# Kernel optimization log

Measured on AMD Instinct MI355X. Metric: run time of the kernel, lower is better.

Reference implementation:

```python
import jax, jax.numpy as jnp
import numpy as np

# Coarse-to-fine lossless 3D segmentation (Seg3dLossless), batch=1, C=1.
RES = [17, 33, 65, 129]          # odd resolutions, stride (RF-1)/(R-1) is integral
RF = RES[-1]
B_MIN, B_MAX = -1.0, 1.0
BAL = 0.5                        # balance_value
N_CONFLICT_ITERS = 2             # fixed unroll of the data-dependent while-loop


def _mlp(pts, w1, b1, w2, b2, w3, b3):
    # query_func: occupancy MLP on normalized (x,y,z) points -> [N]
    h = jax.nn.relu(pts @ w1 + b1)
    h = jax.nn.relu(h @ w2 + b2)
    return jax.nn.sigmoid(h @ w3 + b3)[..., 0]


def _eval_grid(R, w1, b1, w2, b2, w3, b3):
    # batch_eval with align_corners=False: coords2D = (coord + 0.5)/RF, mapped to [B_MIN,B_MAX]
    s = (RF - 1) // (R - 1)
    c = jnp.arange(R, dtype=jnp.float32) * s                 # final-res integer coords
    p = (c + 0.5) / RF * (B_MAX - B_MIN) + B_MIN
    zz, yy, xx = jnp.meshgrid(p, p, p, indexing='ij')        # [D,H,W]
    pts = jnp.stack([xx, yy, zz], axis=-1).reshape(-1, 3)    # (x,y,z) order
    return _mlp(pts, w1, b1, w2, b2, w3, b3).reshape(R, R, R)


def _resize(x, R):
    # trilinear, align_corners=True: out index j -> in coord j*(in-1)/(out-1)
    c = jnp.linspace(0.0, x.shape[0] - 1.0, R)
    zz, yy, xx = jnp.meshgrid(c, c, c, indexing='ij')
    return jax.scipy.ndimage.map_coordinates(x, [zz, yy, xx], order=1, mode='nearest')


def _dilate(m):
    # smooth_conv3x3 (mean filter) followed by >0 == 3x3x3 binary dilation
    f = jax.lax.reduce_window(m.astype(jnp.float32), 0.0, jax.lax.max,
                              (3, 3, 3), (1, 1, 1), 'SAME')
    return f > 0.0


def setup_inputs() -> dict:
    key = jax.random.key(0)
    k1, k2, k3 = jax.random.split(key, 3)
    H = 64
    return {
        'w1': jax.random.normal(k1, (3, H), jnp.float32) * 0.8,
        'b1': jnp.zeros((H,), jnp.float32),
        'w2': jax.random.normal(k2, (H, H), jnp.float32) * (1.0 / np.sqrt(H)),
        'b2': jnp.zeros((H,), jnp.float32),
        'w3': jax.random.normal(k3, (H, 1), jnp.float32) * (1.0 / np.sqrt(H)),
        'b3': jnp.zeros((1,), jnp.float32),
    }


def reference(w1, b1, w2, b2, w3, b3):
    params = (w1, b1, w2, b2, w3, b3)
    # level 0: dense eval on the coarse grid
    occ = _eval_grid(RES[0], *params)                        # [R0,R0,R0]
    s0 = (RF - 1) // (RES[0] - 1)
    calculated = jnp.zeros((RF, RF, RF), bool).at[::s0, ::s0, ::s0].set(True)

    for R in RES[1:]:
        s = (RF - 1) // (R - 1)
        valid = _resize((occ > BAL).astype(jnp.float32), R)  # no-grad mask path
        occ_i = _resize(occ, R)                              # differentiable interp
        boundary = _dilate((valid > 0.0) & (valid < 1.0))
        calc_l = calculated[::s, ::s, ::s]
        boundary = boundary & (~calc_l)                      # skip already-evaluated voxels
        occ_true = _eval_grid(R, *params)                    # query_func at this level
        occ = jnp.where(boundary, occ_true, occ_i)           # scatter of occupancys_topk
        calc_l = calc_l | boundary
        # conflict resolution: re-query 3^3 neighbors of sign-flip voxels
        conflict = boundary & ((occ_i - BAL) * (occ_true - BAL) < 0.0)
        for _ in range(N_CONFLICT_ITERS):
            nbr = _dilate(conflict) & (~calc_l)
            occ_prev = occ
            occ = jnp.where(nbr, occ_true, occ)
            calc_l = calc_l | nbr
            conflict = nbr & ((occ_prev - BAL) * (occ_true - BAL) < 0.0)
        calculated = calculated.at[::s, ::s, ::s].set(calc_l)

    return occ[None, None]                                   # (1, 1, D, H, W)
```

## Files before the change

kernel.cpp:

```cpp
#include <hip/hip_runtime.h>

#define HH 64

static __global__ void k_prep_w2t(const float* __restrict__ w2, float* __restrict__ w2t){
  int t = blockIdx.x * 256 + threadIdx.x;
  w2t[t] = w2[(t & 63) * HH + (t >> 6)];
}

__device__ __forceinline__ void mlp_pair(
    const float* __restrict__ sw1,
    const float* __restrict__ sw2t,
    const float* __restrict__ b2, const float* __restrict__ w3,
    const float* __restrict__ b3,
    float xA, float yA, float zA, float xB, float yB, float zB,
    float& outA, float& outB)
{
  const int ibase = ((threadIdx.x & 63) >> 5) * 32;
  float h1a[32], h1b[32];
  #pragma unroll
  for (int k = 0; k < 32; k += 4){
    const float4 wx = *(const float4*)&sw1[      ibase + k];
    const float4 wy = *(const float4*)&sw1[ 64 + ibase + k];
    const float4 wz = *(const float4*)&sw1[128 + ibase + k];
    const float4 bb = *(const float4*)&sw1[192 + ibase + k];
    h1a[k+0] = fmaxf(fmaf(xA,wx.x,fmaf(yA,wy.x,fmaf(zA,wz.x,bb.x))),0.f);
    h1a[k+1] = fmaxf(fmaf(xA,wx.y,fmaf(yA,wy.y,fmaf(zA,wz.y,bb.y))),0.f);
    h1a[k+2] = fmaxf(fmaf(xA,wx.z,fmaf(yA,wy.z,fmaf(zA,wz.z,bb.z))),0.f);
    h1a[k+3] = fmaxf(fmaf(xA,wx.w,fmaf(yA,wy.w,fmaf(zA,wz.w,bb.w))),0.f);
    h1b[k+0] = fmaxf(fmaf(xB,wx.x,fmaf(yB,wy.x,fmaf(zB,wz.x,bb.x))),0.f);
    h1b[k+1] = fmaxf(fmaf(xB,wx.y,fmaf(yB,wy.y,fmaf(zB,wz.y,bb.y))),0.f);
    h1b[k+2] = fmaxf(fmaf(xB,wx.z,fmaf(yB,wy.z,fmaf(zB,wz.z,bb.z))),0.f);
    h1b[k+3] = fmaxf(fmaf(xB,wx.w,fmaf(yB,wy.w,fmaf(zB,wz.w,bb.w))),0.f);
  }
  float oa = b3[0], ob = oa;
  #pragma unroll 1
  for (int j = 0; j < HH; ++j){
    const float4* wrow = (const float4*)&sw2t[j*HH + ibase];
    float a0 = 0.f, a1 = 0.f, c0 = 0.f, c1 = 0.f;
    #pragma unroll
    for (int q = 0; q < 8; q += 2){
      const float4 w0 = wrow[q];
      const float4 w1q = wrow[q+1];
      a0 = fmaf(h1a[4*q+0], w0.x, a0);
      a0 = fmaf(h1a[4*q+1], w0.y, a0);
      a0 = fmaf(h1a[4*q+2], w0.z, a0);
      a0 = fmaf(h1a[4*q+3], w0.w, a0);
      a1 = fmaf(h1a[4*q+4], w1q.x, a1);
      a1 = fmaf(h1a[4*q+5], w1q.y, a1);
      a1 = fmaf(h1a[4*q+6], w1q.z, a1);
      a1 = fmaf(h1a[4*q+7], w1q.w, a1);
      c0 = fmaf(h1b[4*q+0], w0.x, c0);
      c0 = fmaf(h1b[4*q+1], w0.y, c0);
      c0 = fmaf(h1b[4*q+2], w0.z, c0);
      c0 = fmaf(h1b[4*q+3], w0.w, c0);
      c1 = fmaf(h1b[4*q+4], w1q.x, c1);
      c1 = fmaf(h1b[4*q+5], w1q.y, c1);
      c1 = fmaf(h1b[4*q+6], w1q.z, c1);
      c1 = fmaf(h1b[4*q+7], w1q.w, c1);
    }
    float accA = a0 + a1, accB = c0 + c1;
    accA += __shfl_xor(accA, 32);
    accB += __shfl_xor(accB, 32);
    const float bj = b2[j], wj = w3[j];
    oa = fmaf(fmaxf(accA + bj, 0.f), wj, oa);
    ob = fmaf(fmaxf(accB + bj, 0.f), wj, ob);
  }
  outA = 1.f / (1.f + expf(-oa));
  outB = 1.f / (1.f + expf(-ob));
}

#define STAGE_WEIGHTS()                                            \
  __shared__ float sw1[4*HH];                                      \
  __shared__ float sw2t[HH*HH];                                    \
  {                                                                \
    const int t0 = threadIdx.x;                                    \
    if (t0 < 3*HH) sw1[t0] = w1[t0];                               \
    else sw1[t0] = b1[t0 - 3*HH];                                  \
    const float4* s4 = (const float4*)w2t;                         \
    float4* d4 = (float4*)sw2t;                                    \
    for (int i4 = t0; i4 < HH*HH/4; i4 += 256) d4[i4] = s4[i4];    \
    __syncthreads();                                               \
  }

__device__ __forceinline__ float mlp_eval_s(
    const float* __restrict__ w1, const float* __restrict__ b1,
    const float* __restrict__ w2t, const float* __restrict__ b2,
    const float* __restrict__ w3, const float* __restrict__ b3,
    float x, float y, float z)
{
  float h1[HH];
  #pragma unroll
  for (int i = 0; i < HH; ++i){
    float v = b1[i];
    v = fmaf(x, w1[i],        v);
    v = fmaf(y, w1[HH + i],   v);
    v = fmaf(z, w1[2*HH + i], v);
    h1[i] = fmaxf(v, 0.0f);
  }
  float o = b3[0];
  #pragma unroll 2
  for (int j = 0; j < HH; ++j){
    float acc = b2[j];
    const float* wr = &w2t[j*HH];
    #pragma unroll
    for (int k = 0; k < HH; ++k) acc = fmaf(h1[k], wr[k], acc);
    o = fmaf(fmaxf(acc, 0.0f), w3[j], o);
  }
  return 1.0f / (1.0f + expf(-o));
}

static __global__ __launch_bounds__(256)
__attribute__((amdgpu_waves_per_eu(4,4)))
void k_eval_mlp(
    const float* __restrict__ w1, const float* __restrict__ b1,
    const float* __restrict__ w2t, const float* __restrict__ b2,
    const float* __restrict__ w3, const float* __restrict__ b3,
    float* __restrict__ out, unsigned char* __restrict__ calc1,
    int R, int s)
{
  STAGE_WEIGHTS();
  const unsigned int n = (unsigned int)R * (unsigned int)R * (unsigned int)R;
  const int lane = threadIdx.x & 63;
  const int wid = threadIdx.x >> 6;
  const unsigned int base = blockIdx.x * 256u + (unsigned int)(wid * 64 + (lane & 31));
  const unsigned int pidA = base < n ? base : (n - 1u);
  const unsigned int pB = base + 32u;
  const unsigned int pidB = pB < n ? pB : (n - 1u);
  const float inv129x2 = 2.0f / 129.0f;
  unsigned int cA = pidA % (unsigned int)R, rA = pidA / (unsigned int)R;
  unsigned int cB = pidB % (unsigned int)R, rB = pidB / (unsigned int)R;
  const float xA = ((float)(cA * (unsigned int)s) + 0.5f) * inv129x2 - 1.0f;
  const float yA = ((float)((rA % (unsigned int)R) * (unsigned int)s) + 0.5f) * inv129x2 - 1.0f;
  const float zA = ((float)((rA / (unsigned int)R) * (unsigned int)s) + 0.5f) * inv129x2 - 1.0f;
  const float xB = ((float)(cB * (unsigned int)s) + 0.5f) * inv129x2 - 1.0f;
  const float yB = ((float)((rB % (unsigned int)R) * (unsigned int)s) + 0.5f) * inv129x2 - 1.0f;
  const float zB = ((float)((rB / (unsigned int)R) * (unsigned int)s) + 0.5f) * inv129x2 - 1.0f;
  float oA, oB;
  mlp_pair(sw1, sw2t, b2, w3, b3, xA, yA, zA, xB, yB, zB, oA, oB);
  if ((threadIdx.x & 63) < 32){
    if (base < n){ out[pidA] = oA; if (calc1) calc1[pidA] = 1; }
    if (pB < n)  { out[pidB] = oB; if (calc1) calc1[pidB] = 1; }
  }
}

static __global__ __launch_bounds__(256, 4) void k_eval_dense_mism(
    const float* __restrict__ w1, const float* __restrict__ b1,
    const float* __restrict__ w2t, const float* __restrict__ b2,
    const float* __restrict__ w3, const float* __restrict__ b3,
    const float* __restrict__ occ_i,
    float* __restrict__ out, unsigned char* __restrict__ mism,
    int R, int s)
{
  const unsigned int n = (unsigned int)R * (unsigned int)R * (unsigned int)R;
  unsigned int pid = blockIdx.x * 256u + threadIdx.x;
  if (pid >= n) return;
  const unsigned int c = pid % (unsigned int)R;
  const unsigned int r = pid / (unsigned int)R;
  const unsigned int b = r % (unsigned int)R;
  const unsigned int a = r / (unsigned int)R;
  const float inv129x2 = 2.0f / 129.0f;
  const float x = ((float)(c * (unsigned int)s) + 0.5f) * inv129x2 - 1.0f;
  const float y = ((float)(b * (unsigned int)s) + 0.5f) * inv129x2 - 1.0f;
  const float z = ((float)(a * (unsigned int)s) + 0.5f) * inv129x2 - 1.0f;
  float ot = mlp_eval_s(w1, b1, w2t, b2, w3, b3, x, y, z);
  out[pid] = ot;
  mism[pid] = ((occ_i[pid] - 0.5f) * (ot - 0.5f) < 0.0f) ? (unsigned char)1 : (unsigned char)0;
}

static __global__ __launch_bounds__(256)
__attribute__((amdgpu_waves_per_eu(4,4)))
void k_eval_sparse(
    const float* __restrict__ w1, const float* __restrict__ b1,
    const float* __restrict__ w2t, const float* __restrict__ b2,
    const float* __restrict__ w3, const float* __restrict__ b3,
    const int* __restrict__ idxl, const unsigned int* __restrict__ cnt,
    const float* __restrict__ occ_i,
    float* __restrict__ out, unsigned char* __restrict__ mism,
    int R, int s, unsigned int n)
{
  unsigned int count = *cnt;
  if (count > n) count = n;
  if (blockIdx.x * 256u >= count) return;
  STAGE_WEIGHTS();
  const int lane = threadIdx.x & 63;
  const int wid = threadIdx.x >> 6;
  const unsigned int slotA = blockIdx.x * 256u + (unsigned int)(wid * 64 + (lane & 31));
  const unsigned int slotB = slotA + 32u;
  const bool vA = slotA < count, vB = slotB < count;
  const unsigned int pidA = (unsigned int)idxl[vA ? slotA : 0];
  const unsigned int pidB = (unsigned int)idxl[vB ? slotB : 0];
  const float inv129x2 = 2.0f / 129.0f;
  unsigned int cA = pidA % (unsigned int)R, rA = pidA / (unsigned int)R;
  unsigned int cB = pidB % (unsigned int)R, rB = pidB / (unsigned int)R;
  const float xA = ((float)(cA * (unsigned int)s) + 0.5f) * inv129x2 - 1.0f;
  const float yA = ((float)((rA % (unsigned int)R) * (unsigned int)s) + 0.5f) * inv129x2 - 1.0f;
  const float zA = ((float)((rA / (unsigned int)R) * (unsigned int)s) + 0.5f) * inv129x2 - 1.0f;
  const float xB = ((float)(cB * (unsigned int)s) + 0.5f) * inv129x2 - 1.0f;
  const float yB = ((float)((rB % (unsigned int)R) * (unsigned int)s) + 0.5f) * inv129x2 - 1.0f;
  const float zB = ((float)((rB / (unsigned int)R) * (unsigned int)s) + 0.5f) * inv129x2 - 1.0f;
  float oA, oB;
  mlp_pair(sw1, sw2t, b2, w3, b3, xA, yA, zA, xB, yB, zB, oA, oB);
  if ((threadIdx.x & 63) < 32){
    if (vA){
      out[pidA] = oA;
      mism[pidA] = ((occ_i[pidA] - 0.5f) * (oA - 0.5f) < 0.0f) ? (unsigned char)1 : (unsigned char)0;
    }
    if (vB){
      out[pidB] = oB;
      mism[pidB] = ((occ_i[pidB] - 0.5f) * (oB - 0.5f) < 0.0f) ? (unsigned char)1 : (unsigned char)0;
    }
  }
}

static __global__ __launch_bounds__(256) void k_resize_b0(
    const float* __restrict__ prev,
    const unsigned char* __restrict__ calc_prev,
    float* __restrict__ occ_i, float* __restrict__ occ_out,
    unsigned char* __restrict__ bnd0, unsigned char* __restrict__ calc_out,
    unsigned char* __restrict__ confA, unsigned char* __restrict__ confB,
    unsigned char* __restrict__ upd, int R, int Rp)
{
  const unsigned int n = (unsigned int)R * (unsigned int)R * (unsigned int)R;
  unsigned int gid = blockIdx.x * 256u + threadIdx.x;
  if (gid >= n) return;
  int c = (int)(gid % (unsigned int)R);
  unsigned int r = gid / (unsigned int)R;
  int b = (int)(r % (unsigned int)R);
  int a = (int)(r / (unsigned int)R);
  int a0 = a >> 1, da = a & 1;
  int b0i = b >> 1, db = b & 1;
  int c0 = c >> 1, dc = c & 1;
  float sum = 0.0f;
  int cnt = 0;
  const int tot = (da + 1) * (db + 1) * (dc + 1);
  for (int dz = 0; dz <= da; ++dz)
    for (int dy = 0; dy <= db; ++dy)
      for (int dx = 0; dx <= dc; ++dx){
        float v = prev[((unsigned int)(a0 + dz) * (unsigned int)Rp + (unsigned int)(b0i + dy)) * (unsigned int)Rp + (unsigned int)(c0 + dx)];
        sum += v;
        cnt += (v > 0.5f) ? 1 : 0;
      }
  float oi = sum / (float)tot;
  occ_i[gid] = oi;
  occ_out[gid] = oi;
  bnd0[gid] = (cnt > 0 && cnt < tot) ? 1 : 0;
  calc_out[gid] = ((da | db | dc) == 0)
      ? calc_prev[((unsigned int)a0 * (unsigned int)Rp + (unsigned int)b0i) * (unsigned int)Rp + (unsigned int)c0]
      : (unsigned char)0;
  confA[gid] = 0; confB[gid] = 0; upd[gid] = 0;
}

static __global__ __launch_bounds__(256) void k_resize_boundary(
    const float* __restrict__ prev, const float* __restrict__ occ_true,
    const unsigned char* __restrict__ calc_prev,
    float* __restrict__ occ_i, float* __restrict__ occ_out,
    unsigned char* __restrict__ bnd0,
    unsigned char* __restrict__ mism, unsigned char* __restrict__ calc_out,
    int R, int Rp)
{
  const unsigned int n = (unsigned int)R * (unsigned int)R * (unsigned int)R;
  unsigned int gid = blockIdx.x * 256u + threadIdx.x;
  if (gid >= n) return;
  int c = (int)(gid % (unsigned int)R);
  unsigned int r = gid / (unsigned int)R;
  int b = (int)(r % (unsigned int)R);
  int a = (int)(r / (unsigned int)R);
  int a0 = a >> 1, da = a & 1;
  int b0i = b >> 1, db = b & 1;
  int c0 = c >> 1, dc = c & 1;
  float sum = 0.0f;
  int cnt = 0;
  const int tot = (da + 1) * (db + 1) * (dc + 1);
  for (int dz = 0; dz <= da; ++dz)
    for (int dy = 0; dy <= db; ++dy)
      for (int dx = 0; dx <= dc; ++dx){
        float v = prev[((unsigned int)(a0 + dz) * (unsigned int)Rp + (unsigned int)(b0i + dy)) * (unsigned int)Rp + (unsigned int)(c0 + dx)];
        sum += v;
        cnt += (v > 0.5f) ? 1 : 0;
      }
  float oi = sum / (float)tot;
  occ_i[gid] = oi;
  occ_out[gid] = oi;
  bnd0[gid] = (cnt > 0 && cnt < tot) ? 1 : 0;
  mism[gid] = ((oi - 0.5f) * (occ_true[gid] - 0.5f) < 0.0f) ? 1 : 0;
  calc_out[gid] = ((da | db | dc) == 0)
      ? calc_prev[((unsigned int)a0 * (unsigned int)Rp + (unsigned int)b0i) * (unsigned int)Rp + (unsigned int)c0]
      : (unsigned char)0;
}

static __global__ __launch_bounds__(512) void k_dil7_tiled(
    const unsigned char* __restrict__ in, unsigned char* __restrict__ outp,
    unsigned int* __restrict__ bcnt, int R, int T)
{
  __shared__ unsigned char s0[14*14*14];
  __shared__ unsigned char s1[14*14*8];
  __shared__ unsigned char s2[14*8*8];
  __shared__ unsigned int wc[8];
  const int tile = blockIdx.x;
  const int tz = tile / (T*T);
  const int ty = (tile / T) % T;
  const int tx = tile % T;
  const int bz = tz*8 - 3, by = ty*8 - 3, bx = tx*8 - 3;
  const int t = threadIdx.x;
  for (int i = t; i < 14*14*14; i += 512){
    int lz = i / 196, rr = i % 196, ly = rr / 14, lx = rr % 14;
    int gz = bz + lz, gy = by + ly, gx = bx + lx;
    unsigned char v = 0;
    if (gz >= 0 && gz < R && gy >= 0 && gy < R && gx >= 0 && gx < R)
      v = in[((unsigned int)gz * (unsigned int)R + (unsigned int)gy) * (unsigned int)R + (unsigned int)gx];
    s0[i] = v;
  }
  __syncthreads();
  for (int i = t; i < 14*14*8; i += 512){
    int lz = i / 112, rr = i % 112, ly = rr / 8, lx = rr % 8;
    const unsigned char* p = &s0[lz*196 + ly*14 + lx];
    s1[i] = (unsigned char)(p[0]|p[1]|p[2]|p[3]|p[4]|p[5]|p[6]);
  }
  __syncthreads();
  for (int i = t; i < 14*8*8; i += 512){
    int lz = i / 64, rr = i % 64, ly = rr / 8, lx = rr % 8;
    const unsigned char* p = &s1[lz*112 + ly*8 + lx];
    s2[i] = (unsigned char)(p[0]|p[8]|p[16]|p[24]|p[32]|p[40]|p[48]);
  }
  __syncthreads();
  int lz = t >> 6, ly = (t >> 3) & 7, lx = t & 7;
  const unsigned char* p = &s2[lz*64 + ly*8 + lx];
  int m = p[0]|p[64]|p[128]|p[192]|p[256]|p[320]|p[384];
  int gz = tz*8 + lz, gy = ty*8 + ly, gx = tx*8 + lx;
  bool inb = (gz < R) && (gy < R) && (gx < R);
  if (inb) outp[((unsigned int)gz * (unsigned int)R + (unsigned int)gy) * (unsigned int)R + (unsigned int)gx]
      = (unsigned char)(m ? 1 : 0);
  unsigned long long bm = __ballot(inb && m);
  int w = t >> 6;
  if ((t & 63) == 0) wc[w] = (unsigned int)__popcll(bm);
  __syncthreads();
  if (t == 0) bcnt[blockIdx.x] = wc[0]+wc[1]+wc[2]+wc[3]+wc[4]+wc[5]+wc[6]+wc[7];
}

static __global__ __launch_bounds__(1024) void k_scan(
    unsigned int* __restrict__ bcnt, unsigned int nb, unsigned int* __restrict__ total)
{
  __shared__ unsigned int part[1024];
  const unsigned int t = threadIdx.x;
  const unsigned int chunk = (nb + 1023u) / 1024u;
  const unsigned int beg = t * chunk;
  const unsigned int end = (beg + chunk < nb) ? (beg + chunk) : nb;
  unsigned int s = 0;
  for (unsigned int i = beg; i < end; ++i) s += bcnt[i];
  part[t] = s;
  __syncthreads();
  for (int offd = 1; offd < 1024; offd <<= 1){
    unsigned int v = (t >= (unsigned int)offd) ? part[t - offd] : 0u;
    __syncthreads();
    part[t] += v;
    __syncthreads();
  }
  unsigned int run = (t == 0) ? 0u : part[t - 1];
  for (unsigned int i = beg; i < end; ++i){
    unsigned int v = bcnt[i];
    bcnt[i] = run;
    run += v;
  }
  if (t == 1023) *total = part[1023];
}

static __global__ __launch_bounds__(512) void k_scatter_tiled(
    const unsigned char* __restrict__ cand, const unsigned int* __restrict__ boff,
    int* __restrict__ idxl, int R, int T)
{
  __shared__ unsigned int wbase[8];
  const int tile = blockIdx.x;
  const int tz = tile / (T*T), ty = (tile / T) % T, tx = tile % T;
  const int t = threadIdx.x;
  int lz = t >> 6, ly = (t >> 3) & 7, lx = t & 7;
  int gz = tz*8 + lz, gy = ty*8 + ly, gx = tx*8 + lx;
  bool inb = (gz < R) && (gy < R) && (gx < R);
  int gid = inb ? (int)(((unsigned int)gz * (unsigned int)R + (unsigned int)gy) * (unsigned int)R + (unsigned int)gx) : 0;
  bool pred = inb && (cand[gid] != 0);
  unsigned long long m = __ballot(pred);
  int w = t >> 6, lane = t & 63;
  if (lane == 0) wbase[w] = (unsigned int)__popcll(m);
  __syncthreads();
  if (t == 0){
    unsigned int run = boff[blockIdx.x];
    for (int i = 0; i < 8; ++i){ unsigned int v = wbase[i]; wbase[i] = run; run += v; }
  }
  __syncthreads();
  if (pred){
    int pre = __popcll(m & ((1ull << lane) - 1ull));
    idxl[wbase[w] + (unsigned int)pre] = gid;
  }
}

static __global__ __launch_bounds__(256) void k_dilate_sparse(
    const int* __restrict__ idxl, const unsigned int* __restrict__ cnt,
    const unsigned char* __restrict__ src, const unsigned char* __restrict__ mism,
    unsigned char* __restrict__ calc, unsigned char* __restrict__ conf_out,
    unsigned char* __restrict__ upd, int R, int final_step,
    const float* __restrict__ occ_true, float* __restrict__ occ_out,
    unsigned int n)
{
  unsigned int count = *cnt;
  if (count > n) count = n;
  for (unsigned int slot = blockIdx.x * 256u + threadIdx.x; slot < count;
       slot += gridDim.x * 256u){
    int gid = idxl[slot];
    int c = gid % R;
    int r = gid / R;
    int b = r % R;
    int a = r / R;
    int m = 0;
    for (int dz = -1; dz <= 1; ++dz){
      int az = a + dz; if (az < 0 || az >= R) continue;
      for (int dy = -1; dy <= 1; ++dy){
        int by = b + dy; if (by < 0 || by >= R) continue;
        for (int dx = -1; dx <= 1; ++dx){
          int cx = c + dx; if (cx < 0 || cx >= R) continue;
          m |= src[(az * R + by) * R + cx];
        }
      }
    }
    unsigned char nb = (m && !calc[gid]) ? (unsigned char)1 : (unsigned char)0;
    conf_out[gid] = (nb && mism[gid]) ? (unsigned char)1 : (unsigned char)0;
    unsigned char u = upd[gid];
    if (nb){ calc[gid] = 1; if (!u){ upd[gid] = 1; u = 1; } }
    if (final_step && u) occ_out[gid] = occ_true[gid];
  }
}

static __global__ __launch_bounds__(256) void k_dilate_step(
    const unsigned char* __restrict__ src, const unsigned char* __restrict__ mism,
    unsigned char* __restrict__ calc, unsigned char* __restrict__ conf_out,
    unsigned char* __restrict__ upd, int R, int first, int final_step,
    const float* __restrict__ occ_true, float* __restrict__ occ_out)
{
  const unsigned int n = (unsigned int)R * (unsigned int)R * (unsigned int)R;
  unsigned int gid = blockIdx.x * 256u + threadIdx.x;
  if (gid >= n) return;
  int c = (int)(gid % (unsigned int)R);
  unsigned int r = gid / (unsigned int)R;
  int b = (int)(r % (unsigned int)R);
  int a = (int)(r / (unsigned int)R);
  int m = 0;
  for (int dz = -1; dz <= 1; ++dz){
    int az = a + dz; if (az < 0 || az >= R) continue;
    for (int dy = -1; dy <= 1; ++dy){
      int by = b + dy; if (by < 0 || by >= R) continue;
      for (int dx = -1; dx <= 1; ++dx){
        int cx = c + dx; if (cx < 0 || cx >= R) continue;
        m |= src[((unsigned int)az * (unsigned int)R + (unsigned int)by) * (unsigned int)R + (unsigned int)cx];
      }
    }
  }
  unsigned char nb = (m && !calc[gid]) ? (unsigned char)1 : (unsigned char)0;
  if (nb) calc[gid] = 1;
  conf_out[gid] = (nb && mism[gid]) ? (unsigned char)1 : (unsigned char)0;
  unsigned char u;
  if (first){ u = nb; upd[gid] = nb; }
  else { u = upd[gid]; if (nb && !u){ upd[gid] = 1; u = 1; } }
  if (final_step && u) occ_out[gid] = occ_true[gid];
}

extern "C" void kernel_launch(void* const* d_in, const int* in_sizes, int n_in,
                              void* d_out, int out_size, void* d_ws, size_t ws_size,
                              hipStream_t stream)
{
  const float* w1 = (const float*)d_in[0];
  const float* b1 = (const float*)d_in[1];
  const float* w2 = (const float*)d_in[2];
  const float* b2 = (const float*)d_in[3];
  const float* w3 = (const float*)d_in[4];
  const float* b3 = (const float*)d_in[5];
  float* out = (float*)d_out;

  const int NF = 129 * 129 * 129;
  const int NP = 65 * 65 * 65;
  char* ws = (char*)d_ws;
  size_t off = 0;
  auto alloc = [&](size_t bytes) -> void* {
    void* p = (void*)(ws + off);
    off += (bytes + 255) & ~(size_t)255;
    return p;
  };
  float* f_true  = (float*)alloc((size_t)NF * 4);
  float* f_occi  = (float*)alloc((size_t)NF * 4);
  float* f_prevA = (float*)alloc((size_t)NP * 4);
  float* f_prevB = (float*)alloc((size_t)NP * 4);
  float* f_w2t   = (float*)alloc((size_t)HH * HH * 4);
  int*   i_idx   = (int*)alloc((size_t)NF * 4);
  unsigned int* u_cnt  = (unsigned int*)alloc(256);
  unsigned int* u_bcnt = (unsigned int*)alloc(8448 * 4);
  unsigned char* b_b0    = (unsigned char*)alloc(NF);
  unsigned char* b_mism  = (unsigned char*)alloc(NF);
  unsigned char* b_confA = (unsigned char*)alloc(NF);
  unsigned char* b_confB = (unsigned char*)alloc(NF);
  unsigned char* b_calcA = (unsigned char*)alloc(NF);
  unsigned char* b_calcB = (unsigned char*)alloc(NF);
  unsigned char* b_upd   = (unsigned char*)alloc(NF);
  unsigned char* b_cand  = (unsigned char*)alloc(NF);
  (void)ws_size;

  k_prep_w2t<<<16, 256, 0, stream>>>(w2, f_w2t);

  {
    int R = 17, s = 8;
    int n = R * R * R;
    int blocks = (n + 255) / 256;
    k_eval_mlp<<<blocks, 256, 0, stream>>>(w1, b1, f_w2t, b2, w3, b3, f_prevA, b_calcA, R, s);
  }

  int Rp = 17;
  float* prev = f_prevA;
  unsigned char* calcP = b_calcA;
  unsigned char* calcC = b_calcB;
  for (int li = 1; li <= 3; ++li){
    int R = 2 * Rp - 1;
    int s = 128 / (R - 1);
    unsigned int n = (unsigned int)R * (unsigned int)R * (unsigned int)R;
    int blocks = (int)((n + 255u) / 256u);
    float* occ_out = (li == 3) ? out : ((prev == f_prevA) ? f_prevB : f_prevA);

    if (R == 33){
      k_eval_mlp<<<blocks, 256, 0, stream>>>(w1, b1, f_w2t, b2, w3, b3, f_true, (unsigned char*)nullptr, R, s);
      k_resize_boundary<<<blocks, 256, 0, stream>>>(prev, f_true, calcP, f_occi, occ_out, b_b0, b_mism, calcC, R, Rp);
      k_dilate_step<<<blocks, 256, 0, stream>>>(b_b0,    b_mism, calcC, b_confA, b_upd, R, 1, 0, f_true, occ_out);
      k_dilate_step<<<blocks, 256, 0, stream>>>(b_confA, b_mism, calcC, b_confB, b_upd, R, 0, 0, f_true, occ_out);
      k_dilate_step<<<blocks, 256, 0, stream>>>(b_confB, b_mism, calcC, b_confA, b_upd, R, 0, 1, f_true, occ_out);
    } else if (R == 65){
      k_resize_b0<<<blocks, 256, 0, stream>>>(prev, calcP, f_occi, occ_out, b_b0, calcC,
                                              b_confA, b_confB, b_upd, R, Rp);
      k_eval_dense_mism<<<blocks, 256, 0, stream>>>(w1, b1, f_w2t, b2, w3, b3, f_occi, f_true, b_mism, R, s);
      k_dilate_step<<<blocks, 256, 0, stream>>>(b_b0,    b_mism, calcC, b_confA, b_upd, R, 1, 0, f_true, occ_out);
      k_dilate_step<<<blocks, 256, 0, stream>>>(b_confA, b_mism, calcC, b_confB, b_upd, R, 0, 0, f_true, occ_out);
      k_dilate_step<<<blocks, 256, 0, stream>>>(b_confB, b_mism, calcC, b_confA, b_upd, R, 0, 1, f_true, occ_out);
    } else {
      const int T = (R + 7) / 8;
      const int tblocks = T * T * T;
      k_resize_b0<<<blocks, 256, 0, stream>>>(prev, calcP, f_occi, occ_out, b_b0, calcC,
                                              b_confA, b_confB, b_upd, R, Rp);
      k_dil7_tiled<<<tblocks, 512, 0, stream>>>(b_b0, b_cand, u_bcnt, R, T);
      k_scan<<<1, 1024, 0, stream>>>(u_bcnt, (unsigned int)tblocks, u_cnt);
      k_scatter_tiled<<<tblocks, 512, 0, stream>>>(b_cand, u_bcnt, i_idx, R, T);
      k_eval_sparse<<<blocks, 256, 0, stream>>>(
          w1, b1, f_w2t, b2, w3, b3, i_idx, u_cnt, f_occi, f_true, b_mism, R, s, n);
      int sblocks = blocks < 4096 ? blocks : 4096;
      k_dilate_sparse<<<sblocks, 256, 0, stream>>>(i_idx, u_cnt, b_b0,    b_mism, calcC, b_confA, b_upd, R, 0, f_true, occ_out, n);
      k_dilate_sparse<<<sblocks, 256, 0, stream>>>(i_idx, u_cnt, b_confA, b_mism, calcC, b_confB, b_upd, R, 0, f_true, occ_out, n);
      k_dilate_sparse<<<sblocks, 256, 0, stream>>>(i_idx, u_cnt, b_confB, b_mism, calcC, b_confA, b_upd, R, 1, f_true, occ_out, n);
    }

    prev = occ_out;
    unsigned char* tmpc = calcP; calcP = calcC; calcC = tmpc;
    Rp = R;
  }
  (void)in_sizes; (void)n_in; (void)out_size;
}
```

Measured before the change: 321.4 us.

## Fuse three conflict-dilation passes into one shared-memory tiled kernel per level

```diff
diff --git a/kernel.cpp b/kernel.cpp
--- a/kernel.cpp
+++ b/kernel.cpp
@@ -82,33 +82,6 @@
     __syncthreads();                                               \
   }
 
-__device__ __forceinline__ float mlp_eval_s(
-    const float* __restrict__ w1, const float* __restrict__ b1,
-    const float* __restrict__ w2t, const float* __restrict__ b2,
-    const float* __restrict__ w3, const float* __restrict__ b3,
-    float x, float y, float z)
-{
-  float h1[HH];
-  #pragma unroll
-  for (int i = 0; i < HH; ++i){
-    float v = b1[i];
-    v = fmaf(x, w1[i],        v);
-    v = fmaf(y, w1[HH + i],   v);
-    v = fmaf(z, w1[2*HH + i], v);
-    h1[i] = fmaxf(v, 0.0f);
-  }
-  float o = b3[0];
-  #pragma unroll 2
-  for (int j = 0; j < HH; ++j){
-    float acc = b2[j];
-    const float* wr = &w2t[j*HH];
-    #pragma unroll
-    for (int k = 0; k < HH; ++k) acc = fmaf(h1[k], wr[k], acc);
-    o = fmaf(fmaxf(acc, 0.0f), w3[j], o);
-  }
-  return 1.0f / (1.0f + expf(-o));
-}
-
 static __global__ __launch_bounds__(256)
 __attribute__((amdgpu_waves_per_eu(4,4)))
 void k_eval_mlp(
@@ -141,30 +114,6 @@
     if (base < n){ out[pidA] = oA; if (calc1) calc1[pidA] = 1; }
     if (pB < n)  { out[pidB] = oB; if (calc1) calc1[pidB] = 1; }
   }
-}
-
-static __global__ __launch_bounds__(256, 4) void k_eval_dense_mism(
-    const float* __restrict__ w1, const float* __restrict__ b1,
-    const float* __restrict__ w2t, const float* __restrict__ b2,
-    const float* __restrict__ w3, const float* __restrict__ b3,
-    const float* __restrict__ occ_i,
-    float* __restrict__ out, unsigned char* __restrict__ mism,
-    int R, int s)
-{
-  const unsigned int n = (unsigned int)R * (unsigned int)R * (unsigned int)R;
-  unsigned int pid = blockIdx.x * 256u + threadIdx.x;
-  if (pid >= n) return;
-  const unsigned int c = pid % (unsigned int)R;
-  const unsigned int r = pid / (unsigned int)R;
-  const unsigned int b = r % (unsigned int)R;
-  const unsigned int a = r / (unsigned int)R;
-  const float inv129x2 = 2.0f / 129.0f;
-  const float x = ((float)(c * (unsigned int)s) + 0.5f) * inv129x2 - 1.0f;
-  const float y = ((float)(b * (unsigned int)s) + 0.5f) * inv129x2 - 1.0f;
-  const float z = ((float)(a * (unsigned int)s) + 0.5f) * inv129x2 - 1.0f;
-  float ot = mlp_eval_s(w1, b1, w2t, b2, w3, b3, x, y, z);
-  out[pid] = ot;
-  mism[pid] = ((occ_i[pid] - 0.5f) * (ot - 0.5f) < 0.0f) ? (unsigned char)1 : (unsigned char)0;
 }
 
 static __global__ __launch_bounds__(256)
@@ -217,8 +166,7 @@
     const unsigned char* __restrict__ calc_prev,
     float* __restrict__ occ_i, float* __restrict__ occ_out,
     unsigned char* __restrict__ bnd0, unsigned char* __restrict__ calc_out,
-    unsigned char* __restrict__ confA, unsigned char* __restrict__ confB,
-    unsigned char* __restrict__ upd, int R, int Rp)
+    int R, int Rp)
 {
   const unsigned int n = (unsigned int)R * (unsigned int)R * (unsigned int)R;
   unsigned int gid = blockIdx.x * 256u + threadIdx.x;
@@ -247,7 +195,6 @@
   calc_out[gid] = ((da | db | dc) == 0)
       ? calc_prev[((unsigned int)a0 * (unsigned int)Rp + (unsigned int)b0i) * (unsigned int)Rp + (unsigned int)c0]
       : (unsigned char)0;
-  confA[gid] = 0; confB[gid] = 0; upd[gid] = 0;
 }
 
 static __global__ __launch_bounds__(256) void k_resize_boundary(
@@ -392,73 +339,95 @@
   }
 }
 
-static __global__ __launch_bounds__(256) void k_dilate_sparse(
-    const int* __restrict__ idxl, const unsigned int* __restrict__ cnt,
-    const unsigned char* __restrict__ src, const unsigned char* __restrict__ mism,
-    unsigned char* __restrict__ calc, unsigned char* __restrict__ conf_out,
-    unsigned char* __restrict__ upd, int R, int final_step,
-    const float* __restrict__ occ_true, float* __restrict__ occ_out,
-    unsigned int n)
-{
-  unsigned int count = *cnt;
-  if (count > n) count = n;
-  for (unsigned int slot = blockIdx.x * 256u + threadIdx.x; slot < count;
-       slot += gridDim.x * 256u){
-    int gid = idxl[slot];
-    int c = gid % R;
-    int r = gid / R;
-    int b = r % R;
-    int a = r / R;
+static __global__ __launch_bounds__(512) void k_dilate3_tiled(
+    const unsigned char* __restrict__ b0,
+    const unsigned char* __restrict__ mism,
+    unsigned char* __restrict__ calc,
+    const float* __restrict__ occ_true,
+    float* __restrict__ occ_out,
+    int R, int T)
+{
+  __shared__ unsigned char sC[14*14*14];
+  __shared__ unsigned char sD[14*14*14];
+  __shared__ unsigned char sK[14*14*14];
+  __shared__ unsigned char sM[14*14*14];
+  __shared__ int s_any;
+  const int tile = blockIdx.x;
+  const int tz = tile / (T*T), ty = (tile / T) % T, tx = tile % T;
+  const int bz = tz*8 - 3, by = ty*8 - 3, bx = tx*8 - 3;
+  const int t = threadIdx.x;
+  if (t == 0) s_any = 0;
+  __syncthreads();
+  int any = 0;
+  for (int i = t; i < 2744; i += 512){
+    int lz = i / 196, rr = i % 196, ly = rr / 14, lx = rr % 14;
+    int gz = bz + lz, gy = by + ly, gx = bx + lx;
+    bool in = (gz >= 0 && gz < R && gy >= 0 && gy < R && gx >= 0 && gx < R);
+    unsigned int g = in ? (((unsigned int)gz * (unsigned int)R + (unsigned int)gy) * (unsigned int)R + (unsigned int)gx) : 0u;
+    unsigned char v0 = in ? b0[g] : (unsigned char)0;
+    sC[i] = v0; any |= v0;
+    sK[i] = in ? calc[g] : (unsigned char)1;
+    sM[i] = in ? mism[g] : (unsigned char)0;
+  }
+  if (any) s_any = 1;
+  __syncthreads();
+  if (!s_any) return;
+
+  const int clz = 3 + (t >> 6), cly = 3 + ((t >> 3) & 7), clx = 3 + (t & 7);
+  const int cp = clz*196 + cly*14 + clx;
+  const unsigned char calc0 = sK[cp];
+  __syncthreads();
+
+  for (int i = t; i < 1728; i += 512){
+    int lz = i / 144 + 1, rr = i % 144, ly = rr / 12 + 1, lx = rr % 12 + 1;
+    int p = lz*196 + ly*14 + lx;
     int m = 0;
-    for (int dz = -1; dz <= 1; ++dz){
-      int az = a + dz; if (az < 0 || az >= R) continue;
-      for (int dy = -1; dy <= 1; ++dy){
-        int by = b + dy; if (by < 0 || by >= R) continue;
-        for (int dx = -1; dx <= 1; ++dx){
-          int cx = c + dx; if (cx < 0 || cx >= R) continue;
-          m |= src[(az * R + by) * R + cx];
-        }
-      }
-    }
-    unsigned char nb = (m && !calc[gid]) ? (unsigned char)1 : (unsigned char)0;
-    conf_out[gid] = (nb && mism[gid]) ? (unsigned char)1 : (unsigned char)0;
-    unsigned char u = upd[gid];
-    if (nb){ calc[gid] = 1; if (!u){ upd[gid] = 1; u = 1; } }
-    if (final_step && u) occ_out[gid] = occ_true[gid];
-  }
-}
-
-static __global__ __launch_bounds__(256) void k_dilate_step(
-    const unsigned char* __restrict__ src, const unsigned char* __restrict__ mism,
-    unsigned char* __restrict__ calc, unsigned char* __restrict__ conf_out,
-    unsigned char* __restrict__ upd, int R, int first, int final_step,
-    const float* __restrict__ occ_true, float* __restrict__ occ_out)
-{
-  const unsigned int n = (unsigned int)R * (unsigned int)R * (unsigned int)R;
-  unsigned int gid = blockIdx.x * 256u + threadIdx.x;
-  if (gid >= n) return;
-  int c = (int)(gid % (unsigned int)R);
-  unsigned int r = gid / (unsigned int)R;
-  int b = (int)(r % (unsigned int)R);
-  int a = (int)(r / (unsigned int)R);
-  int m = 0;
-  for (int dz = -1; dz <= 1; ++dz){
-    int az = a + dz; if (az < 0 || az >= R) continue;
-    for (int dy = -1; dy <= 1; ++dy){
-      int by = b + dy; if (by < 0 || by >= R) continue;
-      for (int dx = -1; dx <= 1; ++dx){
-        int cx = c + dx; if (cx < 0 || cx >= R) continue;
-        m |= src[((unsigned int)az * (unsigned int)R + (unsigned int)by) * (unsigned int)R + (unsigned int)cx];
-      }
-    }
-  }
-  unsigned char nb = (m && !calc[gid]) ? (unsigned char)1 : (unsigned char)0;
-  if (nb) calc[gid] = 1;
-  conf_out[gid] = (nb && mism[gid]) ? (unsigned char)1 : (unsigned char)0;
-  unsigned char u;
-  if (first){ u = nb; upd[gid] = nb; }
-  else { u = upd[gid]; if (nb && !u){ upd[gid] = 1; u = 1; } }
-  if (final_step && u) occ_out[gid] = occ_true[gid];
+    #pragma unroll
+    for (int dz = -1; dz <= 1; ++dz)
+      #pragma unroll
+      for (int dy = -1; dy <= 1; ++dy)
+        #pragma unroll
+        for (int dx = -1; dx <= 1; ++dx)
+          m |= sC[p + dz*196 + dy*14 + dx];
+    unsigned char nb = (m && !sK[p]) ? (unsigned char)1 : (unsigned char)0;
+    sD[p] = (nb && sM[p]) ? (unsigned char)1 : (unsigned char)0;
+    if (nb) sK[p] = 1;
+  }
+  __syncthreads();
+  for (int i = t; i < 1000; i += 512){
+    int lz = i / 100 + 2, rr = i % 100, ly = rr / 10 + 2, lx = rr % 10 + 2;
+    int p = lz*196 + ly*14 + lx;
+    int m = 0;
+    #pragma unroll
+    for (int dz = -1; dz <= 1; ++dz)
+      #pragma unroll
+      for (int dy = -1; dy <= 1; ++dy)
+        #pragma unroll
+        for (int dx = -1; dx <= 1; ++dx)
+          m |= sD[p + dz*196 + dy*14 + dx];
+    unsigned char nb = (m && !sK[p]) ? (unsigned char)1 : (unsigned char)0;
+    sC[p] = (nb && sM[p]) ? (unsigned char)1 : (unsigned char)0;
+    if (nb) sK[p] = 1;
+  }
+  __syncthreads();
+  {
+    int m = 0;
+    #pragma unroll
+    for (int dz = -1; dz <= 1; ++dz)
+      #pragma unroll
+      for (int dy = -1; dy <= 1; ++dy)
+        #pragma unroll
+        for (int dx = -1; dx <= 1; ++dx)
+          m |= sC[cp + dz*196 + dy*14 + dx];
+    if (m && !sK[cp]) sK[cp] = 1;
+  }
+  int gz = tz*8 + (clz - 3), gy = ty*8 + (cly - 3), gx = tx*8 + (clx - 3);
+  if (gz < R && gy < R && gx < R){
+    unsigned int g = ((unsigned int)gz * (unsigned int)R + (unsigned int)gy) * (unsigned int)R + (unsigned int)gx;
+    unsigned char cf = sK[cp];
+    calc[g] = cf;
+    if (cf && !calc0) occ_out[g] = occ_true[g];
+  }
 }
 
 extern "C" void kernel_launch(void* const* d_in, const int* in_sizes, int n_in,
@@ -492,11 +461,8 @@
   unsigned int* u_bcnt = (unsigned int*)alloc(8448 * 4);
   unsigned char* b_b0    = (unsigned char*)alloc(NF);
   unsigned char* b_mism  = (unsigned char*)alloc(NF);
-  unsigned char* b_confA = (unsigned char*)alloc(NF);
-  unsigned char* b_confB = (unsigned char*)alloc(NF);
   unsigned char* b_calcA = (unsigned char*)alloc(NF);
   unsigned char* b_calcB = (unsigned char*)alloc(NF);
-  unsigned char* b_upd   = (unsigned char*)alloc(NF);
   unsigned char* b_cand  = (unsigned char*)alloc(NF);
   (void)ws_size;
 
@@ -518,35 +484,22 @@
     int s = 128 / (R - 1);
     unsigned int n = (unsigned int)R * (unsigned int)R * (unsigned int)R;
     int blocks = (int)((n + 255u) / 256u);
+    const int T = (R + 7) / 8;
+    const int tblocks = T * T * T;
     float* occ_out = (li == 3) ? out : ((prev == f_prevA) ? f_prevB : f_prevA);
 
     if (R == 33){
       k_eval_mlp<<<blocks, 256, 0, stream>>>(w1, b1, f_w2t, b2, w3, b3, f_true, (unsigned char*)nullptr, R, s);
       k_resize_boundary<<<blocks, 256, 0, stream>>>(prev, f_true, calcP, f_occi, occ_out, b_b0, b_mism, calcC, R, Rp);
-      k_dilate_step<<<blocks, 256, 0, stream>>>(b_b0,    b_mism, calcC, b_confA, b_upd, R, 1, 0, f_true, occ_out);
-      k_dilate_step<<<blocks, 256, 0, stream>>>(b_confA, b_mism, calcC, b_confB, b_upd, R, 0, 0, f_true, occ_out);
-      k_dilate_step<<<blocks, 256, 0, stream>>>(b_confB, b_mism, calcC, b_confA, b_upd, R, 0, 1, f_true, occ_out);
-    } else if (R == 65){
-      k_resize_b0<<<blocks, 256, 0, stream>>>(prev, calcP, f_occi, occ_out, b_b0, calcC,
-                                              b_confA, b_confB, b_upd, R, Rp);
-      k_eval_dense_mism<<<blocks, 256, 0, stream>>>(w1, b1, f_w2t, b2, w3, b3, f_occi, f_true, b_mism, R, s);
-      k_dilate_step<<<blocks, 256, 0, stream>>>(b_b0,    b_mism, calcC, b_confA, b_upd, R, 1, 0, f_true, occ_out);
-      k_dilate_step<<<blocks, 256, 0, stream>>>(b_confA, b_mism, calcC, b_confB, b_upd, R, 0, 0, f_true, occ_out);
-      k_dilate_step<<<blocks, 256, 0, stream>>>(b_confB, b_mism, calcC, b_confA, b_upd, R, 0, 1, f_true, occ_out);
+      k_dilate3_tiled<<<tblocks, 512, 0, stream>>>(b_b0, b_mism, calcC, f_true, occ_out, R, T);
     } else {
-      const int T = (R + 7) / 8;
-      const int tblocks = T * T * T;
-      k_resize_b0<<<blocks, 256, 0, stream>>>(prev, calcP, f_occi, occ_out, b_b0, calcC,
-                                              b_confA, b_confB, b_upd, R, Rp);
+      k_resize_b0<<<blocks, 256, 0, stream>>>(prev, calcP, f_occi, occ_out, b_b0, calcC, R, Rp);
       k_dil7_tiled<<<tblocks, 512, 0, stream>>>(b_b0, b_cand, u_bcnt, R, T);
       k_scan<<<1, 1024, 0, stream>>>(u_bcnt, (unsigned int)tblocks, u_cnt);
       k_scatter_tiled<<<tblocks, 512, 0, stream>>>(b_cand, u_bcnt, i_idx, R, T);
       k_eval_sparse<<<blocks, 256, 0, stream>>>(
           w1, b1, f_w2t, b2, w3, b3, i_idx, u_cnt, f_occi, f_true, b_mism, R, s, n);
-      int sblocks = blocks < 4096 ? blocks : 4096;
-      k_dilate_sparse<<<sblocks, 256, 0, stream>>>(i_idx, u_cnt, b_b0,    b_mism, calcC, b_confA, b_upd, R, 0, f_true, occ_out, n);
-      k_dilate_sparse<<<sblocks, 256, 0, stream>>>(i_idx, u_cnt, b_confA, b_mism, calcC, b_confB, b_upd, R, 0, f_true, occ_out, n);
-      k_dilate_sparse<<<sblocks, 256, 0, stream>>>(i_idx, u_cnt, b_confB, b_mism, calcC, b_confA, b_upd, R, 1, f_true, occ_out, n);
+      k_dilate3_tiled<<<tblocks, 512, 0, stream>>>(b_b0, b_mism, calcC, f_true, occ_out, R, T);
     }
 
     prev = occ_out;
```

Result: slower. 387.0 us (+20.4%).
